# Performance work log

Hardware: AMD Instinct MI355X
Metric: run time of the kernel (lower is better)

Reference implementation:

```python
import jax, jax.numpy as jnp
import numpy as np

N_CELLS = 64
N_STEPS = 50  # numeric ODE solver steps for the CPAB integration


def _cpab_basis(nc: int) -> np.ndarray:
    """Orthonormal basis of the constrained piecewise-affine velocity space.

    Params layout: p = [a_0, b_0, a_1, b_1, ..., a_{nc-1}, b_{nc-1}], v(x) = a_c x + b_c.
    Constraints: continuity at interior knots, v(0)=0, v(1)=0 (zero_boundary=True).
    """
    L = np.zeros((nc + 1, 2 * nc))
    for k in range(1, nc):
        xk = k / nc
        L[k - 1, 2 * (k - 1):2 * k] = [xk, 1.0]
        L[k - 1, 2 * k:2 * k + 2] = [-xk, -1.0]
    L[nc - 1, 1] = 1.0                       # v(0) = b_0 = 0
    L[nc, 2 * (nc - 1):2 * nc] = [1.0, 1.0]  # v(1) = a_{nc-1} + b_{nc-1} = 0
    _, s, vh = np.linalg.svd(L)
    rank = int(np.sum(s > 1e-10))
    return vh[rank:].T.astype(np.float32)    # (2*nc, nc-1)


def setup_inputs() -> dict:
    key = jax.random.key(0)
    k1, k2 = jax.random.split(key)
    B, S, D = 64, 4096, 128
    d_theta = N_CELLS - 1
    input_seq = jax.random.normal(k1, (B, S, D), dtype=jnp.float32)
    W_loc = 0.05 * jax.random.normal(k2, (D, d_theta), dtype=jnp.float32)
    b_loc = jnp.zeros((d_theta,), dtype=jnp.float32)
    basis = jnp.asarray(_cpab_basis(N_CELLS))  # (2*nc, d_theta)
    return {"input_seq": input_seq, "W_loc": W_loc, "b_loc": b_loc, "basis": basis}


def reference(input_seq, W_loc, b_loc, basis):
    Bsz, S, _ = input_seq.shape
    nc = N_CELLS
    # loc_net: mean pool over sequence + linear -> theta (B, d)
    theta = jnp.mean(input_seq, axis=1) @ W_loc + b_loc            # (B, d)
    # velocity field coefficients per cell: v(x) = a_c x + b_c
    A = (theta @ basis.T).reshape(Bsz, nc, 2)                      # (B, nc, 2)
    a_cells, b_cells = A[..., 0], A[..., 1]
    # uniform_meshgrid([S]) on [0, 1]
    grid = jnp.linspace(0.0, 1.0, S, dtype=input_seq.dtype)
    x0 = jnp.broadcast_to(grid, (Bsz, S))
    dt = 1.0 / N_STEPS

    def step(x, _):
        c = jnp.clip((x * nc).astype(jnp.int32), 0, nc - 1)        # per-point cell lookup
        a = jnp.take_along_axis(a_cells, c, axis=1)
        b = jnp.take_along_axis(b_cells, c, axis=1)
        return x + (a * x + b) * dt, None

    gamma, _ = jax.lax.scan(step, x0, None, length=N_STEPS)
    return gamma                                                   # (B, S)
```

## Files before the change

kernel.cpp:

```cpp
#include <hip/hip_runtime.h>
#include <hip/hip_bf16.h>

constexpr int B       = 64;
constexpr int S       = 4096;
constexpr int D       = 128;
constexpr int NC      = 64;
constexpr int DTH     = 63;
constexpr int NSTEPS  = 50;
constexpr int SPLIT   = 16;
constexpr int SC      = S / SPLIT;

__global__ __launch_bounds__(256) void cpab_reduce(const float* __restrict__ in,
                                                   float* __restrict__ part) {
    const int blk   = blockIdx.x;
    const int b     = blk / SPLIT;
    const int chunk = blk % SPLIT;
    const int t     = threadIdx.x;
    const int d4    = t & 31;
    const int srow  = t >> 5;

    const float4* base = reinterpret_cast<const float4*>(
        in + (size_t)b * S * D + (size_t)chunk * SC * D);

    float4 acc = make_float4(0.f, 0.f, 0.f, 0.f);
    for (int s = srow; s < SC; s += 8) {
        float4 v = base[s * 32 + d4];
        acc.x += v.x; acc.y += v.y; acc.z += v.z; acc.w += v.w;
    }

    __shared__ float4 sm[256];
    sm[t] = acc;
    __syncthreads();

    if (t < 32) {
        float4 a = sm[t];
        #pragma unroll
        for (int r = 1; r < 8; ++r) {
            float4 v = sm[r * 32 + t];
            a.x += v.x; a.y += v.y; a.z += v.z; a.w += v.w;
        }
        reinterpret_cast<float4*>(part + (size_t)(b * SPLIT + chunk) * D)[d4] = a;
    }
}

__global__ __launch_bounds__(128) void cpab_theta(const float* __restrict__ part,
                                                  const float* __restrict__ W,
                                                  const float* __restrict__ bloc,
                                                  const float* __restrict__ basis,
                                                  float* __restrict__ Aout) {
    const int b = blockIdx.x;
    const int t = threadIdx.x;

    __shared__ float s_mean[D];
    __shared__ float s_theta[DTH];

    float tot = 0.f;
    #pragma unroll
    for (int c = 0; c < SPLIT; ++c)
        tot += part[(size_t)(b * SPLIT + c) * D + t];
    s_mean[t] = tot * (1.0f / (float)S);
    __syncthreads();

    if (t < DTH) {
        float th = bloc[t];
        for (int d = 0; d < D; ++d)
            th += s_mean[d] * W[d * DTH + t];
        s_theta[t] = th;
    }
    __syncthreads();

    float acc = 0.f;
    for (int j = 0; j < DTH; ++j)
        acc += s_theta[j] * basis[t * DTH + j];
    Aout[b * 128 + t] = acc;
}

__global__ __launch_bounds__(256) void cpab_warp(const float* __restrict__ Aab,
                                                 float* __restrict__ out) {
    const int blk   = blockIdx.x;
    const int b     = blk >> 4;
    const int chunk = blk & 15;
    const int t     = threadIdx.x;

    __shared__ float ab[128];
    if (t < 128) ab[t] = Aab[b * 128 + t];
    __syncthreads();

    const int s = chunk * 256 + t;
    float x = (float)s * (1.0f / (float)(S - 1));
    const float dt = 1.0f / (float)NSTEPS;

    #pragma unroll
    for (int it = 0; it < NSTEPS; ++it) {
        int c = (int)(x * (float)NC);
        c = c < 0 ? 0 : (c > NC - 1 ? NC - 1 : c);
        float a  = ab[2 * c];
        float bb = ab[2 * c + 1];
        x = x + (a * x + bb) * dt;
    }

    out[(size_t)b * S + s] = x;
}

extern "C" void kernel_launch(void* const* d_in, const int* in_sizes, int n_in,
                              void* d_out, int out_size, void* d_ws, size_t ws_size,
                              hipStream_t stream) {
    const float* in_seq = (const float*)d_in[0];
    const float* W_loc  = (const float*)d_in[1];
    const float* b_loc  = (const float*)d_in[2];
    const float* basis  = (const float*)d_in[3];
    float*       out    = (float*)d_out;

    float* part = out;
    float* Aab  = (float*)d_ws;

    cpab_reduce<<<B * SPLIT, 256, 0, stream>>>(in_seq, part);
    cpab_theta<<<B, 128, 0, stream>>>(part, W_loc, b_loc, basis, Aab);
    cpab_warp<<<B * (S / 256), 256, 0, stream>>>(Aab, out);
}
```

Baseline: 35.47 us.

## Fuse theta projection and ODE warp into one per-batch kernel

Merges the theta/basis projection kernel with the CPAB integration kernel, so each batch's 1024-thread block computes its cell coefficients in shared memory and then integrates 4 points per thread. This removes one kernel launch and the global round trip for the coefficients. The partial sums now go to the workspace instead of the output buffer. In exchange, only 64 blocks run the 50-step integration, which lowers parallelism on a large GPU, and the projection now occupies a 1024-thread block.

```diff
diff --git a/kernel.cpp b/kernel.cpp
--- a/kernel.cpp
+++ b/kernel.cpp
@@ -43,22 +43,25 @@
     }
 }
 
-__global__ __launch_bounds__(128) void cpab_theta(const float* __restrict__ part,
-                                                  const float* __restrict__ W,
-                                                  const float* __restrict__ bloc,
-                                                  const float* __restrict__ basis,
-                                                  float* __restrict__ Aout) {
+__global__ __launch_bounds__(1024) void cpab_batch(const float* __restrict__ part,
+                                                   const float* __restrict__ W,
+                                                   const float* __restrict__ bloc,
+                                                   const float* __restrict__ basis,
+                                                   float* __restrict__ out) {
     const int b = blockIdx.x;
     const int t = threadIdx.x;
 
     __shared__ float s_mean[D];
-    __shared__ float s_theta[DTH];
+    __shared__ float s_theta[64];
+    __shared__ float s_ab[128];
 
-    float tot = 0.f;
-    #pragma unroll
-    for (int c = 0; c < SPLIT; ++c)
-        tot += part[(size_t)(b * SPLIT + c) * D + t];
-    s_mean[t] = tot * (1.0f / (float)S);
+    if (t < D) {
+        float tot = 0.f;
+        #pragma unroll
+        for (int c = 0; c < SPLIT; ++c)
+            tot += part[(size_t)(b * SPLIT + c) * D + t];
+        s_mean[t] = tot * (1.0f / (float)S);
+    }
     __syncthreads();
 
     if (t < DTH) {
@@ -69,37 +72,45 @@
     }
     __syncthreads();
 
-    float acc = 0.f;
-    for (int j = 0; j < DTH; ++j)
-        acc += s_theta[j] * basis[t * DTH + j];
-    Aout[b * 128 + t] = acc;
-}
-
-__global__ __launch_bounds__(256) void cpab_warp(const float* __restrict__ Aab,
-                                                 float* __restrict__ out) {
-    const int blk   = blockIdx.x;
-    const int b     = blk >> 4;
-    const int chunk = blk & 15;
-    const int t     = threadIdx.x;
-
-    __shared__ float ab[128];
-    if (t < 128) ab[t] = Aab[b * 128 + t];
+    if (t < 128) {
+        float acc = 0.f;
+        for (int j = 0; j < DTH; ++j)
+            acc += s_theta[j] * basis[t * DTH + j];
+        s_ab[t] = acc;
+    }
     __syncthreads();
 
-    const int s = chunk * 256 + t;
-    float x = (float)s * (1.0f / (float)(S - 1));
     const float dt = 1.0f / (float)NSTEPS;
+    float x0 = (float)(t)          * (1.0f / (float)(S - 1));
+    float x1 = (float)(t + 1024)   * (1.0f / (float)(S - 1));
+    float x2 = (float)(t + 2048)   * (1.0f / (float)(S - 1));
+    float x3 = (float)(t + 3072)   * (1.0f / (float)(S - 1));
 
     #pragma unroll
     for (int it = 0; it < NSTEPS; ++it) {
-        int c = (int)(x * (float)NC);
-        c = c < 0 ? 0 : (c > NC - 1 ? NC - 1 : c);
-        float a  = ab[2 * c];
-        float bb = ab[2 * c + 1];
-        x = x + (a * x + bb) * dt;
+        int c0 = (int)(x0 * (float)NC);
+        int c1 = (int)(x1 * (float)NC);
+        int c2 = (int)(x2 * (float)NC);
+        int c3 = (int)(x3 * (float)NC);
+        c0 = c0 < 0 ? 0 : (c0 > NC - 1 ? NC - 1 : c0);
+        c1 = c1 < 0 ? 0 : (c1 > NC - 1 ? NC - 1 : c1);
+        c2 = c2 < 0 ? 0 : (c2 > NC - 1 ? NC - 1 : c2);
+        c3 = c3 < 0 ? 0 : (c3 > NC - 1 ? NC - 1 : c3);
+        float a0 = s_ab[2 * c0], b0 = s_ab[2 * c0 + 1];
+        float a1 = s_ab[2 * c1], b1 = s_ab[2 * c1 + 1];
+        float a2 = s_ab[2 * c2], b2 = s_ab[2 * c2 + 1];
+        float a3 = s_ab[2 * c3], b3 = s_ab[2 * c3 + 1];
+        x0 = x0 + (a0 * x0 + b0) * dt;
+        x1 = x1 + (a1 * x1 + b1) * dt;
+        x2 = x2 + (a2 * x2 + b2) * dt;
+        x3 = x3 + (a3 * x3 + b3) * dt;
     }
 
-    out[(size_t)b * S + s] = x;
+    float* ob = out + (size_t)b * S;
+    ob[t]        = x0;
+    ob[t + 1024] = x1;
+    ob[t + 2048] = x2;
+    ob[t + 3072] = x3;
 }
 
 extern "C" void kernel_launch(void* const* d_in, const int* in_sizes, int n_in,
@@ -111,10 +122,8 @@
     const float* basis  = (const float*)d_in[3];
     float*       out    = (float*)d_out;
 
-    float* part = out;
-    float* Aab  = (float*)d_ws;
+    float* part = (float*)d_ws;
 
     cpab_reduce<<<B * SPLIT, 256, 0, stream>>>(in_seq, part);
-    cpab_theta<<<B, 128, 0, stream>>>(part, W_loc, b_loc, basis, Aab);
-    cpab_warp<<<B * (S / 256), 256, 0, stream>>>(Aab, out);
+    cpab_batch<<<B, 1024, 0, stream>>>(part, W_loc, b_loc, basis, out);
 }
```

Result: slower. 40.58 us (+14.4%).

## Fuse theta projection into reduce and warp kernels, drop middle launch

Applied to the files above, without the earlier changes.

The three-kernel pipeline becomes two. Each reduce block now projects its partial column sums through W_loc into a 63-wide partial theta. Each warp block sums the per-chunk partial thetas, adds the bias and scale, and computes the per-cell coefficients from the basis before integrating. This removes one kernel launch and the serialized small theta kernel. In exchange the W matvec is repeated in every reduce block and the basis projection is repeated in all 16 warp blocks per batch.

```diff
diff --git a/kernel.cpp b/kernel.cpp
--- a/kernel.cpp
+++ b/kernel.cpp
@@ -10,8 +10,11 @@
 constexpr int SPLIT   = 16;
 constexpr int SC      = S / SPLIT;
 
-__global__ __launch_bounds__(256) void cpab_reduce(const float* __restrict__ in,
-                                                   float* __restrict__ part) {
+constexpr int THC_LD  = 64;
+
+__global__ __launch_bounds__(256) void cpab_reduce_theta(const float* __restrict__ in,
+                                                         const float* __restrict__ W,
+                                                         float* __restrict__ thc) {
     const int blk   = blockIdx.x;
     const int b     = blk / SPLIT;
     const int chunk = blk % SPLIT;
@@ -29,6 +32,7 @@
     }
 
     __shared__ float4 sm[256];
+    __shared__ float  s_col[D];
     sm[t] = acc;
     __syncthreads();
 
@@ -39,51 +43,46 @@
             float4 v = sm[r * 32 + t];
             a.x += v.x; a.y += v.y; a.z += v.z; a.w += v.w;
         }
-        reinterpret_cast<float4*>(part + (size_t)(b * SPLIT + chunk) * D)[d4] = a;
+        reinterpret_cast<float4*>(s_col)[t] = a;
+    }
+    __syncthreads();
+
+    if (t < DTH) {
+        float th = 0.f;
+        #pragma unroll 8
+        for (int d = 0; d < D; ++d)
+            th += s_col[d] * W[d * DTH + t];
+        thc[(size_t)(b * SPLIT + chunk) * THC_LD + t] = th;
     }
 }
 
-__global__ __launch_bounds__(128) void cpab_theta(const float* __restrict__ part,
-                                                  const float* __restrict__ W,
+__global__ __launch_bounds__(256) void cpab_warp2(const float* __restrict__ thc,
                                                   const float* __restrict__ bloc,
                                                   const float* __restrict__ basis,
-                                                  float* __restrict__ Aout) {
-    const int b = blockIdx.x;
-    const int t = threadIdx.x;
-
-    __shared__ float s_mean[D];
-    __shared__ float s_theta[DTH];
-
-    float tot = 0.f;
-    #pragma unroll
-    for (int c = 0; c < SPLIT; ++c)
-        tot += part[(size_t)(b * SPLIT + c) * D + t];
-    s_mean[t] = tot * (1.0f / (float)S);
-    __syncthreads();
-
-    if (t < DTH) {
-        float th = bloc[t];
-        for (int d = 0; d < D; ++d)
-            th += s_mean[d] * W[d * DTH + t];
-        s_theta[t] = th;
-    }
-    __syncthreads();
-
-    float acc = 0.f;
-    for (int j = 0; j < DTH; ++j)
-        acc += s_theta[j] * basis[t * DTH + j];
-    Aout[b * 128 + t] = acc;
-}
-
-__global__ __launch_bounds__(256) void cpab_warp(const float* __restrict__ Aab,
-                                                 float* __restrict__ out) {
+                                                  float* __restrict__ out) {
     const int blk   = blockIdx.x;
     const int b     = blk >> 4;
     const int chunk = blk & 15;
     const int t     = threadIdx.x;
 
-    __shared__ float ab[128];
-    if (t < 128) ab[t] = Aab[b * 128 + t];
+    __shared__ float s_theta[64];
+    __shared__ float s_ab[128];
+
+    if (t < DTH) {
+        float acc = 0.f;
+        #pragma unroll
+        for (int c = 0; c < SPLIT; ++c)
+            acc += thc[(size_t)(b * SPLIT + c) * THC_LD + t];
+        s_theta[t] = bloc[t] + acc * (1.0f / (float)S);
+    }
+    __syncthreads();
+
+    if (t < 128) {
+        float acc = 0.f;
+        for (int j = 0; j < DTH; ++j)
+            acc += s_theta[j] * basis[t * DTH + j];
+        s_ab[t] = acc;
+    }
     __syncthreads();
 
     const int s = chunk * 256 + t;
@@ -94,8 +93,8 @@
     for (int it = 0; it < NSTEPS; ++it) {
         int c = (int)(x * (float)NC);
         c = c < 0 ? 0 : (c > NC - 1 ? NC - 1 : c);
-        float a  = ab[2 * c];
-        float bb = ab[2 * c + 1];
+        float a  = s_ab[2 * c];
+        float bb = s_ab[2 * c + 1];
         x = x + (a * x + bb) * dt;
     }
 
@@ -111,10 +110,8 @@
     const float* basis  = (const float*)d_in[3];
     float*       out    = (float*)d_out;
 
-    float* part = out;
-    float* Aab  = (float*)d_ws;
+    float* thc = (float*)d_ws;
 
-    cpab_reduce<<<B * SPLIT, 256, 0, stream>>>(in_seq, part);
-    cpab_theta<<<B, 128, 0, stream>>>(part, W_loc, b_loc, basis, Aab);
-    cpab_warp<<<B * (S / 256), 256, 0, stream>>>(Aab, out);
+    cpab_reduce_theta<<<B * SPLIT, 256, 0, stream>>>(in_seq, W_loc, thc);
+    cpab_warp2<<<B * (S / 256), 256, 0, stream>>>(thc, b_loc, basis, out);
 }
```

After: 35.95 us. About the same (+1.3%).
